# Kernel optimization log

Hardware: AMD Instinct MI355X
Metric: run time of the kernel (lower is better)

Reference implementation:

```python
import jax, jax.numpy as jnp
import numpy as np

B, S, D, H, DFF = 4, 2048, 1024, 16, 4096
DK = D // H
EPS = 1e-5


def _linear_params(key, fan_in, fan_out):
    kw, kb = jax.random.split(key)
    bound = 1.0 / np.sqrt(fan_in)
    w = jax.random.uniform(kw, (fan_in, fan_out), minval=-bound, maxval=bound, dtype=jnp.float32)
    b = jax.random.uniform(kb, (fan_out,), minval=-bound, maxval=bound, dtype=jnp.float32)
    return w, b


def setup_inputs() -> dict:
    key = jax.random.key(0)
    ks = jax.random.split(key, 8)
    x = jax.random.normal(ks[0], (B, S, D), dtype=jnp.float32)
    mask = jnp.ones((B, 1, 1, S), dtype=jnp.int32)
    wq, bq = _linear_params(ks[1], D, D)
    wk, bk = _linear_params(ks[2], D, D)
    wv, bv = _linear_params(ks[3], D, D)
    wo, bo = _linear_params(ks[4], D, D)
    w1, b1 = _linear_params(ks[5], D, DFF)
    w2, b2 = _linear_params(ks[6], DFF, D)
    g1 = jnp.ones((D,), jnp.float32); be1 = jnp.zeros((D,), jnp.float32)
    g2 = jnp.ones((D,), jnp.float32); be2 = jnp.zeros((D,), jnp.float32)
    return {"x": x, "mask": mask, "wq": wq, "bq": bq, "wk": wk, "bk": bk,
            "wv": wv, "bv": bv, "wo": wo, "bo": bo, "w1": w1, "b1": b1,
            "w2": w2, "b2": b2, "g1": g1, "be1": be1, "g2": g2, "be2": be2}


def _layernorm(x, g, b):
    mu = jnp.mean(x, axis=-1, keepdims=True)
    var = jnp.mean(jnp.square(x - mu), axis=-1, keepdims=True)
    return (x - mu) * jax.lax.rsqrt(var + EPS) * g + b


def reference(x, mask, wq, bq, wk, bk, wv, bv, wo, bo, w1, b1, w2, b2, g1, be1, g2, be2):
    # Multi-head self-attention
    q = (x @ wq + bq).reshape(B, S, H, DK).transpose(0, 2, 1, 3)  # b h s d
    k = (x @ wk + bk).reshape(B, S, H, DK).transpose(0, 2, 1, 3)
    v = (x @ wv + bv).reshape(B, S, H, DK).transpose(0, 2, 1, 3)
    scores = jnp.einsum('bhqd,bhkd->bhqk', q, k) / np.sqrt(DK)
    scores = jnp.where(mask == 0, jnp.float32(-1e9), scores)
    attn = jax.nn.softmax(scores, axis=-1)
    ctx = jnp.einsum('bhqk,bhkd->bhqd', attn, v)
    ctx = ctx.transpose(0, 2, 1, 3).reshape(B, S, D)
    attn_out = ctx @ wo + bo
    # Dropout is identity in eval mode
    out1 = _layernorm(x + attn_out, g1, be1)
    ffn = jax.nn.relu(out1 @ w1 + b1) @ w2 + b2
    out2 = _layernorm(out1 + ffn, g2, be2)
    return out2
```

## Files before the change

### kernel.cpp

```cpp
#include <hip/hip_runtime.h>
#include <cstdint>
#include <cstddef>

typedef __bf16 bf16_t;
typedef __bf16 bf16x4 __attribute__((ext_vector_type(4)));
typedef __bf16 bf16x8 __attribute__((ext_vector_type(8)));
typedef float f32x4 __attribute__((ext_vector_type(4)));

#define GLD_LDS16(g, l)                                                                   \
  __builtin_amdgcn_global_load_lds((const __attribute__((address_space(1))) void*)(g),   \
                                   (__attribute__((address_space(3))) void*)(l), 16, 0, 0)

__device__ __forceinline__ int swbits(int row) {
  return ((row ^ (row >> 3)) & 7) << 4;
}
__device__ __forceinline__ int swz(int row, int colbyte) {
  return row * 128 + (colbyte ^ swbits(row));
}

__global__ __launch_bounds__(256) void transpose_cvt_k(const float* __restrict__ src,
                                                       bf16_t* __restrict__ dst, int R, int C) {
  __shared__ float t[64][65];
  const int tid = threadIdx.x;
  const int tr = blockIdx.y * 64, tc = blockIdx.x * 64;
  const int r0 = tid >> 2, c0 = (tid & 3) * 16;
#pragma unroll
  for (int i = 0; i < 16; i += 4) {
    float4 v = *(const float4*)(src + (size_t)(tr + r0) * C + tc + c0 + i);
    t[r0][c0 + i] = v.x; t[r0][c0 + i + 1] = v.y;
    t[r0][c0 + i + 2] = v.z; t[r0][c0 + i + 3] = v.w;
  }
  __syncthreads();
  bf16x8 w0, w1;
#pragma unroll
  for (int i = 0; i < 8; ++i) {
    w0[i] = (bf16_t)t[c0 + i][r0];
    w1[i] = (bf16_t)t[c0 + 8 + i][r0];
  }
  *(bf16x8*)(dst + (size_t)(tc + r0) * R + tr + c0) = w0;
  *(bf16x8*)(dst + (size_t)(tc + r0) * R + tr + c0 + 8) = w1;
}

__global__ __launch_bounds__(256) void cvt_k(const float* __restrict__ in,
                                             bf16_t* __restrict__ out) {
  const size_t i = ((size_t)blockIdx.x * 256 + threadIdx.x) * 8;
  float4 a = *(const float4*)(in + i);
  float4 b = *(const float4*)(in + i + 4);
  bf16x8 o;
  o[0] = (bf16_t)a.x; o[1] = (bf16_t)a.y; o[2] = (bf16_t)a.z; o[3] = (bf16_t)a.w;
  o[4] = (bf16_t)b.x; o[5] = (bf16_t)b.y; o[6] = (bf16_t)b.z; o[7] = (bf16_t)b.w;
  *(bf16x8*)(out + i) = o;
}

template <int EPI>
__global__ __launch_bounds__(256) void gemm_bt(
    const bf16_t* __restrict__ A, const bf16_t* __restrict__ Bt,
    const float* __restrict__ bias0, const bf16_t* __restrict__ res,
    bf16_t* __restrict__ out0, int N, int K) {
  __shared__ __align__(16) bf16_t As[128][64];
  __shared__ __align__(16) bf16_t Bs[128][64];
  const int tid = threadIdx.x, lane = tid & 63, wave = tid >> 6;
  const int wm = wave >> 1, wn = wave & 1;
  const int tile_m = blockIdx.y * 128, tile_n = blockIdx.x * 128;

  f32x4 acc[4][4];
#pragma unroll
  for (int i = 0; i < 4; ++i)
#pragma unroll
    for (int j = 0; j < 4; ++j)
#pragma unroll
      for (int c = 0; c < 4; ++c) acc[i][j][c] = 0.f;

  for (int k0 = 0; k0 < K; k0 += 64) {
    __syncthreads();
#pragma unroll
    for (int j = 0; j < 4; ++j) {
      const int c = j * 256 + tid;
      GLD_LDS16(A + (size_t)(tile_m + (c >> 3)) * K + k0 + (c & 7) * 8,
                (char*)As + j * 4096 + wave * 1024);
      GLD_LDS16(Bt + (size_t)(tile_n + (c >> 3)) * K + k0 + (c & 7) * 8,
                (char*)Bs + j * 4096 + wave * 1024);
    }
    __syncthreads();
#pragma unroll
    for (int kk = 0; kk < 2; ++kk) {
      bf16x8 a[4], b[4];
#pragma unroll
      for (int i = 0; i < 4; ++i)
        a[i] = *(const bf16x8*)&As[wm * 64 + i * 16 + (lane & 15)][kk * 32 + (lane >> 4) * 8];
#pragma unroll
      for (int i = 0; i < 4; ++i)
        b[i] = *(const bf16x8*)&Bs[wn * 64 + i * 16 + (lane & 15)][kk * 32 + (lane >> 4) * 8];
#pragma unroll
      for (int mi = 0; mi < 4; ++mi)
#pragma unroll
        for (int ni = 0; ni < 4; ++ni)
          acc[mi][ni] = __builtin_amdgcn_mfma_f32_16x16x32_bf16(a[mi], b[ni], acc[mi][ni], 0, 0, 0);
    }
  }

#pragma unroll
  for (int mi = 0; mi < 4; ++mi) {
#pragma unroll
    for (int ni = 0; ni < 4; ++ni) {
      const int col = tile_n + wn * 64 + ni * 16 + (lane & 15);
      const int rbase = tile_m + wm * 64 + mi * 16 + (lane >> 4) * 4;
      const float bv = bias0[col];
#pragma unroll
      for (int r = 0; r < 4; ++r) {
        const int row = rbase + r;
        float v = acc[mi][ni][r] + bv;
        if constexpr (EPI == 1) v += (float)res[(size_t)row * N + col];
        out0[(size_t)row * N + col] = (bf16_t)v;
      }
    }
  }
}

template <int EPI>
__global__ __launch_bounds__(512, 1) void gemm256(
    const bf16_t* __restrict__ A, const bf16_t* __restrict__ Bt,
    const float* __restrict__ bias0, const float* __restrict__ bias1,
    const float* __restrict__ bias2,
    bf16_t* __restrict__ out0, bf16_t* __restrict__ out1, bf16_t* __restrict__ out2,
    int N, int K) {
  extern __shared__ __align__(16) char lds[];
  const int tid = threadIdx.x, lane = tid & 63, wave = tid >> 6;
  const int fr = lane & 15, hi = lane >> 4;
  const int wm = wave >> 2, wn = wave & 3;
  const int tile_n = blockIdx.x * 256, tile_m = blockIdx.y * 256;
  const int NT = K >> 6;
  const int s_r = tid >> 3, s_cb = (tid & 7) * 16;

  f32x4 acc[8][4];
#pragma unroll
  for (int m = 0; m < 8; ++m)
#pragma unroll
    for (int n = 0; n < 4; ++n)
#pragma unroll
      for (int c = 0; c < 4; ++c) acc[m][n][c] = 0.f;

#define STAGE256(t, cbuf)                                                                  \
  do {                                                                                     \
    const size_t k0_ = (size_t)(t) * 64;                                                   \
    _Pragma("unroll") for (int h_ = 0; h_ < 2; ++h_)                                       \
        _Pragma("unroll") for (int is_ = 0; is_ < 2; ++is_) {                              \
      const int r_ = is_ * 64 + s_r;                                                       \
      GLD_LDS16(A + (size_t)(tile_m + h_ * 128 + r_) * K + k0_ + ((s_cb ^ swbits(r_)) >> 1),\
                lds + (cbuf)*65536 + h_ * 16384 + is_ * 8192 + wave * 1024);               \
    }                                                                                      \
    _Pragma("unroll") for (int h_ = 0; h_ < 2; ++h_)                                       \
        _Pragma("unroll") for (int is_ = 0; is_ < 2; ++is_) {                              \
      const int r_ = is_ * 64 + s_r;                                                       \
      GLD_LDS16(Bt + (size_t)(tile_n + h_ * 128 + r_) * K + k0_ + ((s_cb ^ swbits(r_)) >> 1),\
                lds + (cbuf)*65536 + 32768 + h_ * 16384 + is_ * 8192 + wave * 1024);       \
    }                                                                                      \
  } while (0)

  STAGE256(0, 0);
  for (int t = 0; t < NT; ++t) {
    const int c = t & 1;
    if (t + 1 < NT) {
      STAGE256(t + 1, c ^ 1);
      asm volatile("s_waitcnt vmcnt(8)" ::: "memory");
    } else {
      asm volatile("s_waitcnt vmcnt(0)" ::: "memory");
    }
    __builtin_amdgcn_s_barrier();
    __builtin_amdgcn_sched_barrier(0);

    bf16x8 bfrag[4][2];
#pragma unroll
    for (int n = 0; n < 4; ++n)
#pragma unroll
      for (int kk = 0; kk < 2; ++kk)
        bfrag[n][kk] = *(const bf16x8*)(lds + c * 65536 + 32768 + (wn >> 1) * 16384 +
                                        swz((wn & 1) * 64 + n * 16 + fr, kk * 64 + hi * 16));
#pragma unroll
    for (int p = 0; p < 4; ++p) {
      bf16x8 afrag[2][2];
#pragma unroll
      for (int mm = 0; mm < 2; ++mm)
#pragma unroll
        for (int kk = 0; kk < 2; ++kk)
          afrag[mm][kk] = *(const bf16x8*)(lds + c * 65536 + wm * 16384 +
                                           swz((p * 2 + mm) * 16 + fr, kk * 64 + hi * 16));
      __builtin_amdgcn_sched_barrier(0);
      __builtin_amdgcn_s_barrier();
      __builtin_amdgcn_s_setprio(1);
#pragma unroll
      for (int mm = 0; mm < 2; ++mm)
#pragma unroll
        for (int n = 0; n < 4; ++n)
#pragma unroll
          for (int kk = 0; kk < 2; ++kk)
            acc[p * 2 + mm][n] = __builtin_amdgcn_mfma_f32_16x16x32_bf16(
                afrag[mm][kk], bfrag[n][kk], acc[p * 2 + mm][n], 0, 0, 0);
      __builtin_amdgcn_s_setprio(0);
      __builtin_amdgcn_s_barrier();
      __builtin_amdgcn_sched_barrier(0);
    }
  }
#undef STAGE256

#pragma unroll
  for (int m = 0; m < 8; ++m) {
#pragma unroll
    for (int n = 0; n < 4; ++n) {
      const int col = tile_n + wn * 64 + n * 16 + fr;
      const int rbase = tile_m + wm * 128 + m * 16 + hi * 4;
      if constexpr (EPI == 0) {
        const int which = tile_n >> 10;
        const float* bp = which == 0 ? bias0 : (which == 1 ? bias1 : bias2);
        bf16_t* op = which == 0 ? out0 : (which == 1 ? out1 : out2);
        const float sca = which == 0 ? 0.18033688f : 1.0f;
        const int cc = col & 1023, h = cc >> 6, dk = cc & 63;
        const float bv = bp[cc];
#pragma unroll
        for (int r = 0; r < 4; ++r) {
          const int row = rbase + r, bb = row >> 11, ss = row & 2047;
          op[(((size_t)bb * 16 + h) * 2048 + ss) * 64 + dk] = (bf16_t)((acc[m][n][r] + bv) * sca);
        }
      } else {
        const float bv = bias0[col];
#pragma unroll
        for (int r = 0; r < 4; ++r) {
          const int row = rbase + r;
          float v = acc[m][n][r] + bv;
          if constexpr (EPI == 2) v = v > 0.f ? v : 0.f;
          out0[(size_t)row * N + col] = (bf16_t)v;
        }
      }
    }
  }
}

__global__ __launch_bounds__(256) void attn_k(
    const bf16_t* __restrict__ Q, const bf16_t* __restrict__ Kb, const bf16_t* __restrict__ Vb,
    const int* __restrict__ mask, bf16_t* __restrict__ ctxout) {
  __shared__ __align__(16) char Qs[16384];
  __shared__ __align__(16) char Ks[2][8192];
  __shared__ __align__(16) char Vt[2][8192];
  __shared__ __align__(16) char Ps[16384];
  const int tid = threadIdx.x, lane = tid & 63, wave = tid >> 6;
  const int fr = lane & 15, hi = lane >> 4;
  const int qt = blockIdx.x, bh = blockIdx.y, b = bh >> 4, h = bh & 15;
  const bf16_t* qbase = Q + ((size_t)bh * 2048 + qt * 128) * 64;
  const bf16_t* kbase = Kb + (size_t)bh * 2048 * 64;
  const bf16_t* vbase = Vb + (size_t)bh * 2048 * 64;
  const int* mbase = mask + b * 2048;

  const int src_r = tid >> 3;
  const int src_cb = (tid & 7) * 16;

#pragma unroll
  for (int j = 0; j < 4; ++j) {
    const int c = j * 256 + tid, rr = c >> 3, cb = (c & 7) * 16;
    GLD_LDS16(qbase + rr * 64 + ((cb ^ swbits(rr)) >> 1), Qs + j * 4096 + wave * 1024);
  }
#pragma unroll
  for (int j = 0; j < 2; ++j) {
    const int rr = j * 32 + src_r;
    GLD_LDS16(kbase + rr * 64 + ((src_cb ^ swbits(rr)) >> 1), Ks[0] + j * 4096 + wave * 1024);
  }
  {
    bf16x8 v0 = *(const bf16x8*)(vbase + (size_t)(tid >> 3) * 64 + (tid & 7) * 8);
    bf16x8 v1 = *(const bf16x8*)(vbase + (size_t)(32 + (tid >> 3)) * 64 + (tid & 7) * 8);
    const int kp0 = tid >> 3, kp1 = 32 + (tid >> 3), d0 = (tid & 7) * 8;
#pragma unroll
    for (int i = 0; i < 8; ++i) {
      *(bf16_t*)(Vt[0] + swz(d0 + i, kp0 * 2)) = v0[i];
      *(bf16_t*)(Vt[0] + swz(d0 + i, kp1 * 2)) = v1[i];
    }
  }
  __syncthreads();

  f32x4 ctx[2][4];
  float l_prt[2][4];
#pragma unroll
  for (int mi = 0; mi < 2; ++mi)
#pragma unroll
    for (int r = 0; r < 4; ++r) {
      l_prt[mi][r] = 0.f;
#pragma unroll
      for (int di = 0; di < 4; ++di) ctx[mi][di][r] = 0.f;
    }

  for (int kt = 0; kt < 32; ++kt) {
    const int cur = kt & 1;
    bf16x8 vr0, vr1;
    if (kt < 31) {
#pragma unroll
      for (int j = 0; j < 2; ++j) {
        const int rr = j * 32 + src_r;
        GLD_LDS16(kbase + (size_t)(kt + 1) * 4096 + rr * 64 + ((src_cb ^ swbits(rr)) >> 1),
                  Ks[cur ^ 1] + j * 4096 + wave * 1024);
      }
      vr0 = *(const bf16x8*)(vbase + (size_t)(kt + 1) * 4096 + (size_t)(tid >> 3) * 64 +
                             (tid & 7) * 8);
      vr1 = *(const bf16x8*)(vbase + (size_t)(kt + 1) * 4096 + (size_t)(32 + (tid >> 3)) * 64 +
                             (tid & 7) * 8);
    }
    int mv[4];
#pragma unroll
    for (int ni = 0; ni < 4; ++ni) mv[ni] = mbase[kt * 64 + ni * 16 + fr];

    f32x4 sc[2][4];
#pragma unroll
    for (int mi = 0; mi < 2; ++mi)
#pragma unroll
      for (int ni = 0; ni < 4; ++ni)
#pragma unroll
        for (int c = 0; c < 4; ++c) sc[mi][ni][c] = 0.f;
#pragma unroll
    for (int kk = 0; kk < 2; ++kk) {
      bf16x8 aq[2], kb_[4];
#pragma unroll
      for (int mi = 0; mi < 2; ++mi)
        aq[mi] = *(const bf16x8*)(Qs + swz(wave * 32 + mi * 16 + fr, kk * 64 + hi * 16));
#pragma unroll
      for (int ni = 0; ni < 4; ++ni)
        kb_[ni] = *(const bf16x8*)(Ks[cur] + swz(ni * 16 + fr, kk * 64 + hi * 16));
#pragma unroll
      for (int mi = 0; mi < 2; ++mi)
#pragma unroll
        for (int ni = 0; ni < 4; ++ni)
          sc[mi][ni] = __builtin_amdgcn_mfma_f32_16x16x32_bf16(aq[mi], kb_[ni], sc[mi][ni], 0, 0, 0);
    }

#pragma unroll
    for (int mi = 0; mi < 2; ++mi) {
#pragma unroll
      for (int r = 0; r < 4; ++r) {
        float rsum = 0.f;
#pragma unroll
        for (int ni = 0; ni < 4; ++ni) {
          const float p = mv[ni] ? exp2f(sc[mi][ni][r]) : 0.f;
          sc[mi][ni][r] = p;
          rsum += p;
        }
        l_prt[mi][r] += rsum;
      }
      const int qrow = wave * 32 + mi * 16 + hi * 4;
#pragma unroll
      for (int ni = 0; ni < 4; ++ni)
#pragma unroll
        for (int r = 0; r < 4; ++r)
          *(bf16_t*)(Ps + swz(qrow + r, (ni * 16 + fr) * 2)) = (bf16_t)sc[mi][ni][r];
    }
    asm volatile("s_waitcnt lgkmcnt(0)" ::: "memory");
    __builtin_amdgcn_sched_barrier(0);

#pragma unroll
    for (int kk = 0; kk < 2; ++kk) {
      bf16x8 pa[2], vv[4];
#pragma unroll
      for (int mi = 0; mi < 2; ++mi)
        pa[mi] = *(const bf16x8*)(Ps + swz(wave * 32 + mi * 16 + fr, kk * 64 + hi * 16));
#pragma unroll
      for (int di = 0; di < 4; ++di)
        vv[di] = *(const bf16x8*)(Vt[cur] + swz(di * 16 + fr, kk * 64 + hi * 16));
#pragma unroll
      for (int mi = 0; mi < 2; ++mi)
#pragma unroll
        for (int di = 0; di < 4; ++di)
          ctx[mi][di] =
              __builtin_amdgcn_mfma_f32_16x16x32_bf16(pa[mi], vv[di], ctx[mi][di], 0, 0, 0);
    }

    if (kt < 31) {
      const int kp0 = tid >> 3, kp1 = 32 + (tid >> 3), d0 = (tid & 7) * 8;
#pragma unroll
      for (int i = 0; i < 8; ++i) {
        *(bf16_t*)(Vt[cur ^ 1] + swz(d0 + i, kp0 * 2)) = vr0[i];
        *(bf16_t*)(Vt[cur ^ 1] + swz(d0 + i, kp1 * 2)) = vr1[i];
      }
    }
    __syncthreads();
  }

#pragma unroll
  for (int mi = 0; mi < 2; ++mi)
#pragma unroll
    for (int r = 0; r < 4; ++r) {
      float l = l_prt[mi][r];
#pragma unroll
      for (int d = 1; d < 16; d <<= 1) l += __shfl_xor(l, d);
      const float inv = 1.f / l;
      const int srow = qt * 128 + wave * 32 + mi * 16 + hi * 4 + r;
#pragma unroll
      for (int di = 0; di < 4; ++di) {
        const int col = h * 64 + di * 16 + fr;
        ctxout[((size_t)b * 2048 + srow) * 1024 + col] = (bf16_t)(ctx[mi][di][r] * inv);
      }
    }
}

template <int F32OUT>
__global__ __launch_bounds__(256) void ln_k(const bf16_t* __restrict__ in,
                                            const float* __restrict__ g,
                                            const float* __restrict__ be,
                                            void* __restrict__ out) {
  __shared__ float red[8];
  const int tid = threadIdx.x;
  const size_t row = blockIdx.x;
  bf16x4 v4 = *(const bf16x4*)(in + row * 1024 + tid * 4);
  const float f0 = (float)v4[0], f1 = (float)v4[1], f2 = (float)v4[2], f3 = (float)v4[3];
  float s = f0 + f1 + f2 + f3;
  float s2 = f0 * f0 + f1 * f1 + f2 * f2 + f3 * f3;
#pragma unroll
  for (int d = 1; d < 64; d <<= 1) { s += __shfl_xor(s, d); s2 += __shfl_xor(s2, d); }
  if ((tid & 63) == 0) { red[tid >> 6] = s; red[4 + (tid >> 6)] = s2; }
  __syncthreads();
  s = red[0] + red[1] + red[2] + red[3];
  s2 = red[4] + red[5] + red[6] + red[7];
  const float mu = s * (1.f / 1024.f);
  const float var = s2 * (1.f / 1024.f) - mu * mu;
  const float rs = rsqrtf(var + 1e-5f);
  float4 gv = *(const float4*)(g + tid * 4);
  float4 bv = *(const float4*)(be + tid * 4);
  const float r0 = (f0 - mu) * rs * gv.x + bv.x;
  const float r1 = (f1 - mu) * rs * gv.y + bv.y;
  const float r2 = (f2 - mu) * rs * gv.z + bv.z;
  const float r3 = (f3 - mu) * rs * gv.w + bv.w;
  if constexpr (F32OUT) {
    float4 o = {r0, r1, r2, r3};
    *(float4*)((float*)out + row * 1024 + tid * 4) = o;
  } else {
    bf16x4 o;
    o[0] = (bf16_t)r0; o[1] = (bf16_t)r1; o[2] = (bf16_t)r2; o[3] = (bf16_t)r3;
    *(bf16x4*)((bf16_t*)out + row * 1024 + tid * 4) = o;
  }
}

extern "C" void kernel_launch(void* const* d_in, const int* in_sizes, int n_in,
                              void* d_out, int out_size, void* d_ws, size_t ws_size,
                              hipStream_t stream) {
  const float* x    = (const float*)d_in[0];
  const int*   mask = (const int*)d_in[1];
  const float* wq = (const float*)d_in[2];
  const float* bq = (const float*)d_in[3];
  const float* wk = (const float*)d_in[4];
  const float* bk = (const float*)d_in[5];
  const float* wv = (const float*)d_in[6];
  const float* bv = (const float*)d_in[7];
  const float* wo = (const float*)d_in[8];
  const float* bo = (const float*)d_in[9];
  const float* w1 = (const float*)d_in[10];
  const float* b1 = (const float*)d_in[11];
  const float* w2 = (const float*)d_in[12];
  const float* b2 = (const float*)d_in[13];
  const float* g1  = (const float*)d_in[14];
  const float* be1 = (const float*)d_in[15];
  const float* g2  = (const float*)d_in[16];
  const float* be2 = (const float*)d_in[17];

  char* wsb = (char*)d_ws;
  bf16_t* S0  = (bf16_t*)wsb;
  bf16_t* XB  = (bf16_t*)(wsb + 8388608);
  bf16_t* QB  = (bf16_t*)(wsb + 25165824);
  bf16_t* KB  = (bf16_t*)(wsb + 41943040);
  bf16_t* VB  = (bf16_t*)(wsb + 58720256);
  bf16_t* CTX = (bf16_t*)(wsb + 75497472);
  bf16_t* FFN = QB;
  bf16_t* Y   = (bf16_t*)(wsb + 92274688);
  bf16_t* O1  = (bf16_t*)(wsb + 109051904);

  (void)hipFuncSetAttribute((const void*)gemm256<0>,
                            hipFuncAttributeMaxDynamicSharedMemorySize, 131072);
  (void)hipFuncSetAttribute((const void*)gemm256<2>,
                            hipFuncAttributeMaxDynamicSharedMemorySize, 131072);

  dim3 blk(256);
  cvt_k<<<4096, blk, 0, stream>>>(x, XB);
  transpose_cvt_k<<<dim3(16, 16), blk, 0, stream>>>(wq, S0, 1024, 1024);
  transpose_cvt_k<<<dim3(16, 16), blk, 0, stream>>>(wk, S0 + 1048576, 1024, 1024);
  transpose_cvt_k<<<dim3(16, 16), blk, 0, stream>>>(wv, S0 + 2097152, 1024, 1024);
  gemm256<0><<<dim3(12, 32), 512, 131072, stream>>>(XB, S0, bq, bk, bv,
                                                    QB, KB, VB, 3072, 1024);
  transpose_cvt_k<<<dim3(16, 16), blk, 0, stream>>>(wo, S0, 1024, 1024);
  attn_k<<<dim3(16, 64), blk, 0, stream>>>(QB, KB, VB, mask, CTX);
  gemm_bt<1><<<dim3(8, 64), blk, 0, stream>>>(CTX, S0, bo, XB, Y, 1024, 1024);
  transpose_cvt_k<<<dim3(64, 16), blk, 0, stream>>>(w1, S0, 1024, 4096);
  ln_k<0><<<8192, blk, 0, stream>>>(Y, g1, be1, O1);
  gemm256<2><<<dim3(16, 32), 512, 131072, stream>>>(O1, S0, b1, nullptr, nullptr,
                                                    FFN, nullptr, nullptr, 4096, 1024);
  transpose_cvt_k<<<dim3(16, 64), blk, 0, stream>>>(w2, S0, 4096, 1024);
  gemm_bt<1><<<dim3(8, 64), blk, 0, stream>>>(FFN, S0, b2, O1, Y, 1024, 4096);
  ln_k<1><<<8192, blk, 0, stream>>>(Y, g2, be2, d_out);
}
```

Measured before the change: 498.7 us.

## Double-buffer A fragments in GEMM loop and precompute mask tile flags in attention

In the GEMM main loop, A-fragment LDS reads are now double-buffered across the four sub-steps, with the next fragment loaded while the current MFMAs run. The per-substep barriers and sched_barriers are removed and replaced by a single barrier per K-tile. In attention, a per-wave bitmask of key tiles containing any masked entries is built up front with ballots. Mask loads and selects are then skipped for clean tiles, and masked scores become -1e9 before exp2. This trades fewer barriers and mask loads for more register pressure, and it changes how the waves stay in sync.

```diff
diff --git a/kernel.cpp b/kernel.cpp
--- a/kernel.cpp
+++ b/kernel.cpp
@@ -167,7 +167,6 @@
       asm volatile("s_waitcnt vmcnt(0)" ::: "memory");
     }
     __builtin_amdgcn_s_barrier();
-    __builtin_amdgcn_sched_barrier(0);
 
     bf16x8 bfrag[4][2];
 #pragma unroll
@@ -176,17 +175,24 @@
       for (int kk = 0; kk < 2; ++kk)
         bfrag[n][kk] = *(const bf16x8*)(lds + c * 65536 + 32768 + (wn >> 1) * 16384 +
                                         swz((wn & 1) * 64 + n * 16 + fr, kk * 64 + hi * 16));
+    bf16x8 af[2][2][2];
+#pragma unroll
+    for (int mm = 0; mm < 2; ++mm)
+#pragma unroll
+      for (int kk = 0; kk < 2; ++kk)
+        af[0][mm][kk] = *(const bf16x8*)(lds + c * 65536 + wm * 16384 +
+                                         swz(mm * 16 + fr, kk * 64 + hi * 16));
 #pragma unroll
     for (int p = 0; p < 4; ++p) {
-      bf16x8 afrag[2][2];
-#pragma unroll
-      for (int mm = 0; mm < 2; ++mm)
-#pragma unroll
-        for (int kk = 0; kk < 2; ++kk)
-          afrag[mm][kk] = *(const bf16x8*)(lds + c * 65536 + wm * 16384 +
-                                           swz((p * 2 + mm) * 16 + fr, kk * 64 + hi * 16));
-      __builtin_amdgcn_sched_barrier(0);
-      __builtin_amdgcn_s_barrier();
+      if (p < 3) {
+#pragma unroll
+        for (int mm = 0; mm < 2; ++mm)
+#pragma unroll
+          for (int kk = 0; kk < 2; ++kk)
+            af[(p + 1) & 1][mm][kk] =
+                *(const bf16x8*)(lds + c * 65536 + wm * 16384 +
+                                 swz(((p + 1) * 2 + mm) * 16 + fr, kk * 64 + hi * 16));
+      }
       __builtin_amdgcn_s_setprio(1);
 #pragma unroll
       for (int mm = 0; mm < 2; ++mm)
@@ -195,11 +201,10 @@
 #pragma unroll
           for (int kk = 0; kk < 2; ++kk)
             acc[p * 2 + mm][n] = __builtin_amdgcn_mfma_f32_16x16x32_bf16(
-                afrag[mm][kk], bfrag[n][kk], acc[p * 2 + mm][n], 0, 0, 0);
+                af[p & 1][mm][kk], bfrag[n][kk], acc[p * 2 + mm][n], 0, 0, 0);
       __builtin_amdgcn_s_setprio(0);
-      __builtin_amdgcn_s_barrier();
-      __builtin_amdgcn_sched_barrier(0);
-    }
+    }
+    __builtin_amdgcn_s_barrier();
   }
 #undef STAGE256
 
@@ -273,6 +278,11 @@
       *(bf16_t*)(Vt[0] + swz(d0 + i, kp1 * 2)) = v1[i];
     }
   }
+  unsigned dirty = 0;
+#pragma unroll 1
+  for (int kt2 = 0; kt2 < 32; ++kt2) {
+    if (__ballot(mbase[kt2 * 64 + lane] == 0) != 0ull) dirty |= 1u << kt2;
+  }
   __syncthreads();
 
   f32x4 ctx[2][4];
@@ -301,9 +311,6 @@
       vr1 = *(const bf16x8*)(vbase + (size_t)(kt + 1) * 4096 + (size_t)(32 + (tid >> 3)) * 64 +
                              (tid & 7) * 8);
     }
-    int mv[4];
-#pragma unroll
-    for (int ni = 0; ni < 4; ++ni) mv[ni] = mbase[kt * 64 + ni * 16 + fr];
 
     f32x4 sc[2][4];
 #pragma unroll
@@ -328,6 +335,19 @@
           sc[mi][ni] = __builtin_amdgcn_mfma_f32_16x16x32_bf16(aq[mi], kb_[ni], sc[mi][ni], 0, 0, 0);
     }
 
+    if (dirty & (1u << kt)) {
+      int mv[4];
+#pragma unroll
+      for (int ni = 0; ni < 4; ++ni) mv[ni] = mbase[kt * 64 + ni * 16 + fr];
+#pragma unroll
+      for (int mi = 0; mi < 2; ++mi)
+#pragma unroll
+        for (int ni = 0; ni < 4; ++ni)
+#pragma unroll
+          for (int r = 0; r < 4; ++r)
+            sc[mi][ni][r] = mv[ni] ? sc[mi][ni][r] : -1e9f;
+    }
+
 #pragma unroll
     for (int mi = 0; mi < 2; ++mi) {
 #pragma unroll
@@ -335,7 +355,7 @@
         float rsum = 0.f;
 #pragma unroll
         for (int ni = 0; ni < 4; ++ni) {
-          const float p = mv[ni] ? exp2f(sc[mi][ni][r]) : 0.f;
+          const float p = exp2f(sc[mi][ni][r]);
           sc[mi][ni][r] = p;
           rsum += p;
         }
```

New measurement: 497.7 us. Within noise of the previous version (-0.2%).
